# Optimization experiments

Measured on AMD Instinct MI355X. Metric: run time of the kernel, lower is better.

## Reference

```python
import jax, jax.numpy as jnp
import numpy as np

B, N, NB, E, H, A, K, D = 32, 512, 10, 1024, 256, 82, 4, 3


def setup_inputs() -> dict:
    key = jax.random.key(0)
    ks = iter(jax.random.split(key, 64))
    f = lambda shape: jax.random.normal(next(ks), shape, jnp.float32) * 0.05
    inp = {
        "atom_fea": jax.random.normal(next(ks), (B, N, A), jnp.float32),
        "bond_fea": jax.random.normal(next(ks), (B, E, 6), jnp.float32),
        "d_anb": jax.random.randint(next(ks), (B, N, NB), 0, N),
        "d_bnb": jax.random.randint(next(ks), (B, N, NB), 0, E),
        "d_nbs_mask": (jax.random.uniform(next(ks), (B, N, NB)) < 0.8).astype(jnp.float32),
        "d_mask": (jax.random.uniform(next(ks), (B, N)) < 0.9).astype(jnp.float32),
        "Wv": f((A, H)), "bv": f((H,)),
        "Wa_main": f((D, K, H, H)), "ba_main": f((D, K, H)),
        "Wa_super": f((D, K, H, H)), "ba_super": f((D, K, H)),
        "Wm": f((D, K, H, H)), "bm": f((D, K, H)),
        "Wbmm": f((D, K, H)), "bbmm": f((D, K)),
        "Wm2s": f((D, K * H, H)), "bm2s": f((D, H)),
        "Ws2m": f((D, H, H)), "bs2m": f((D, H)),
        "Wsup": f((D, H, H)), "bsup": f((D, H)),
        "Wzm1": f((D, H, H)), "bzm1": f((D, H)),
        "Wzm2": f((D, H, H)), "bzm2": f((D, H)),
        "Wzs1": f((D, H, H)), "bzs1": f((D, H)),
        "Wzs2": f((D, H, H)), "bzs2": f((D, H)),
        "Wu2": f((D, H + 6, H)), "bu2": f((D, H)),
        "Wu1": f((D, 2 * H, H)), "bu1": f((D, H)),
    }
    return inp


def mask_softmax(a, mask):
    a_max = jnp.max(a, -1, keepdims=True)
    e = jnp.exp(a - a_max) * mask
    return e / (jnp.sum(e, -1, keepdims=True) + 1e-6)


def _forward(atom_fea, bond_fea, d_nbs_mask, d_mask,
             Wv, bv, Wa_main, ba_main, Wa_super, ba_super, Wm, bm, Wbmm, bbmm,
             Wm2s, bm2s, Ws2m, bs2m, Wsup, bsup,
             Wzm1, bzm1, Wzm2, bzm2, Wzs1, bzs1, Wzs2, bzs2,
             Wu2, bu2, Wu1, bu1, d_anb, d_bnb):
    Bn = atom_fea.shape[0]
    bidx = jnp.arange(Bn)[:, None, None]
    # vertex embedding (default leaky_relu slope 0.01)
    vf = jax.nn.leaky_relu(atom_fea @ Wv + bv, 0.01)            # [B,N,H]
    sf = jnp.sum(vf * d_mask[:, :, None], axis=1, keepdims=True)  # [B,1,H]
    mask3 = d_nbs_mask[..., None]                               # [B,N,NB,1]
    for d in range(D):
        # --- multi-head main->super attention (vectorized over heads k) ---
        a_main = jnp.tanh(jnp.einsum('bnh,khj->bknj', vf, Wa_main[d]) + ba_main[d][None, :, None, :])
        a_super = jnp.tanh(jnp.einsum('boh,khj->bkoj', sf, Wa_super[d]) + ba_super[d][None, :, None, :])
        a = jnp.einsum('bknh,kh->bkn', a_main * a_super, Wbmm[d]) + bbmm[d][None, :, None]
        attn = mask_softmax(a, d_mask[:, None, :])               # [B,K,N]
        mvf = jnp.einsum('bnh,khj->bknj', vf, Wm[d]) + bm[d][None, :, None, :]
        m2s = jnp.einsum('bkn,bknh->bkh', attn, mvf).reshape(Bn, 1, K * H)
        main_to_super = jnp.tanh(m2s @ Wm2s[d] + bm2s[d])        # [B,1,H]
        # --- wln unit: gather neighbors, MLP, masked sum (slope 0.1) ---
        vnei = vf[bidx, d_anb]                                   # [B,N,NB,H]
        enei = bond_fea[bidx, d_bnb]                             # [B,N,NB,6]
        lnei = jnp.concatenate([vnei, enei], -1)                 # [B,N,NB,H+6]
        nei = jax.nn.leaky_relu(lnei @ Wu2[d] + bu2[d], 0.1)
        nei = jnp.sum(nei * mask3, axis=2)                       # [B,N,H]
        main_self = jax.nn.leaky_relu(jnp.concatenate([vf, nei], -1) @ Wu1[d] + bu1[d], 0.1)
        # --- GRU-style gated updates ---
        super_to_main = jnp.tanh(sf @ Ws2m[d] + bs2m[d])         # [B,1,H]
        super_self = jnp.tanh(sf @ Wsup[d] + bsup[d])            # [B,1,H]
        z_main = jax.nn.sigmoid(main_self @ Wzm1[d] + bzm1[d] + super_to_main @ Wzm2[d] + bzm2[d])
        vf = (1 - z_main) * main_self + z_main * super_to_main
        z_sup = jax.nn.sigmoid(super_self @ Wzs1[d] + bzs1[d] + main_to_super @ Wzs2[d] + bzs2[d])
        sf = (1 - z_sup) * super_self + z_sup * main_to_super    # [B,1,H]; sum over dim 1 is a no-op
    return vf, sf


def reference(atom_fea, bond_fea, d_anb, d_bnb, d_nbs_mask, d_mask,
              Wv, bv, Wa_main, ba_main, Wa_super, ba_super, Wm, bm, Wbmm, bbmm,
              Wm2s, bm2s, Ws2m, bs2m, Wsup, bsup,
              Wzm1, bzm1, Wzm2, bzm2, Wzs1, bzs1, Wzs2, bzs2,
              Wu2, bu2, Wu1, bu1):
    return _forward(atom_fea, bond_fea, d_nbs_mask, d_mask,
                    Wv, bv, Wa_main, ba_main, Wa_super, ba_super, Wm, bm, Wbmm, bbmm,
                    Wm2s, bm2s, Ws2m, bs2m, Wsup, bsup,
                    Wzm1, bzm1, Wzm2, bzm2, Wzs1, bzs1, Wzs2, bzs2,
                    Wu2, bu2, Wu1, bu1, d_anb, d_bnb)
```

## Files before the change

### kernel.cpp

```cpp
#include <hip/hip_runtime.h>
#include <hip/hip_bf16.h>

#define B_ 32
#define N_ 512
#define NB_ 10
#define E_ 1024
#define H_ 256
#define A_ 82
#define K_ 4
#define D_ 3
#define M_ (B_*N_)

typedef unsigned short u16;
typedef __attribute__((ext_vector_type(8))) short bf16x8;
typedef __attribute__((ext_vector_type(4))) float f32x4;

__device__ __forceinline__ float b2f(u16 u){
    unsigned int x = ((unsigned int)u) << 16;
    return __builtin_bit_cast(float, x);
}
__device__ __forceinline__ u16 f2b(float f){
    unsigned int x = __builtin_bit_cast(unsigned int, f);
    unsigned int lsb = (x >> 16) & 1u;
    x += 0x7fffu + lsb;
    return (u16)(x >> 16);
}
__device__ __forceinline__ float sigmoidf_(float x){ return 1.f/(1.f+expf(-x)); }

static constexpr int CVT_N[31] = {
    B_*E_*6, B_*N_*NB_, B_*N_,
    A_*H_, H_,
    D_*K_*H_*H_, D_*K_*H_, D_*K_*H_*H_, D_*K_*H_,
    D_*K_*H_*H_, D_*K_*H_, D_*K_*H_, D_*K_,
    D_*K_*H_*H_, D_*H_, D_*H_*H_, D_*H_,
    D_*H_*H_, D_*H_, D_*H_*H_, D_*H_,
    D_*H_*H_, D_*H_, D_*H_*H_, D_*H_,
    D_*H_*H_, D_*H_, D_*(H_+6)*H_, D_*H_,
    D_*2*H_*H_, D_*H_
};
struct Offs { long v[32]; };
static constexpr Offs mk_offs(){
    Offs o{}; o.v[0]=0;
    for(int i=0;i<31;i++) o.v[i+1]=o.v[i]+CVT_N[i];
    return o;
}
static constexpr Offs CVT_OFF = mk_offs();

struct Ptrs { const void* p[31]; };

__global__ void k_detect(const unsigned short* __restrict__ wv_raw, int* __restrict__ flag){
    float v = b2f(wv_raw[threadIdx.x]);
    bool plaus = (v==v) && (fabsf(v) < 100.0f);
    unsigned long long m = __ballot(plaus);
    if (threadIdx.x==0) *flag = (m == ~0ULL) ? 1 : 0;
}

__global__ void k_cvt(Ptrs ptrs, float* __restrict__ dst, const int* __restrict__ flag){
    int t = blockIdx.y;
    int n = CVT_N[t];
    int i4 = blockIdx.x*256 + threadIdx.x;
    if (i4*4 >= n) return;
    const void* src = ptrs.p[t];
    float4 o;
    if (*flag){
        ushort4 u = ((const ushort4*)src)[i4];
        o.x=b2f(u.x); o.y=b2f(u.y); o.z=b2f(u.z); o.w=b2f(u.w);
    } else {
        o = ((const float4*)src)[i4];
    }
    *(float4*)(dst + CVT_OFF.v[t] + (size_t)i4*4) = o;
}

__global__ void k_embed(const u16* __restrict__ atom, const float* __restrict__ Wv,
                        const float* __restrict__ bv, float* __restrict__ vf,
                        const int* __restrict__ flag){
    __shared__ float arow[A_];
    int row = blockIdx.x; int j = threadIdx.x;
    if (j < A_){
        if (*flag) arow[j] = b2f(atom[(size_t)row*A_ + j]);
        else       arow[j] = ((const float*)atom)[(size_t)row*A_ + j];
    }
    __syncthreads();
    float acc = bv[j];
    for(int a=0;a<A_;a++) acc += arow[a]*Wv[a*H_ + j];
    vf[(size_t)row*H_ + j] = acc > 0.f ? acc : 0.01f*acc;
}

__global__ void k_sf0(const float* __restrict__ vf, const float* __restrict__ dmask,
                      float* __restrict__ sf){
    int b = blockIdx.x, h = threadIdx.x;
    __shared__ float mk[N_];
    for(int n=threadIdx.x;n<N_;n+=256) mk[n] = dmask[b*N_+n];
    __syncthreads();
    float s=0.f;
    #pragma unroll 8
    for(int n=0;n<N_;n++) s += mk[n]*vf[((size_t)b*N_+n)*H_ + h];
    sf[b*H_+h]=s;
}

__global__ void k_s1(int d, const float* __restrict__ sf,
    const float* __restrict__ Was, const float* __restrict__ bas,
    const float* __restrict__ Wbmm,
    const float* __restrict__ Ws2m, const float* __restrict__ bs2m,
    const float* __restrict__ Wsup, const float* __restrict__ bsup,
    float* __restrict__ asw, float* __restrict__ s2m, float* __restrict__ ssf)
{
    int b = blockIdx.x, m = blockIdx.y, j = threadIdx.x;
    __shared__ float sfl[H_];
    sfl[j] = sf[b*H_+j];
    __syncthreads();
    const float* W; float bias;
    if (m < 4){ W = Was + (size_t)(d*K_+m)*H_*H_; bias = bas[(d*K_+m)*H_+j]; }
    else if (m==4){ W = Ws2m + (size_t)d*H_*H_; bias = bs2m[d*H_+j]; }
    else { W = Wsup + (size_t)d*H_*H_; bias = bsup[d*H_+j]; }
    float acc = bias;
    #pragma unroll 8
    for(int h=0;h<H_;h++) acc += sfl[h]*W[h*H_+j];
    float v = tanhf(acc);
    if (m < 4) asw[(b*K_+m)*H_+j] = v * Wbmm[(d*K_+m)*H_+j];
    else if (m==4) s2m[b*H_+j] = v;
    else ssf[b*H_+j] = v;
}

__global__ void k_s2(int d, const float* __restrict__ s2m,
    const float* __restrict__ Wzm2, const float* __restrict__ bzm2,
    float* __restrict__ stm2p)
{
    int b=blockIdx.x, c=blockIdx.y, j=threadIdx.x;
    __shared__ float xl[64];
    if (j<64) xl[j] = s2m[b*H_ + c*64 + j];
    __syncthreads();
    const float* W = Wzm2 + (size_t)d*H_*H_ + (size_t)(c*64)*H_;
    float acc = (c==0) ? bzm2[d*H_+j] : 0.f;
    #pragma unroll 8
    for(int h=0;h<64;h++) acc += xl[h]*W[h*H_+j];
    stm2p[((size_t)c*B_+b)*H_+j] = acc;
}

__device__ __forceinline__ void mfma_core_f32(const float* __restrict__ A,
    const float* __restrict__ W, f32x4 acc[2][8],
    u16* __restrict__ Als, u16* __restrict__ Ws)
{
    const int LSA = 40, LSW = 40;
    int tid = threadIdx.x;
    int lane = tid & 63, wave = tid >> 6;
    int wy = wave >> 1, wx = wave & 1;
    int quad = lane >> 4, l15 = lane & 15;
    #pragma unroll
    for(int mt=0;mt<2;mt++)
        #pragma unroll
        for(int nt=0;nt<8;nt++) acc[mt][nt] = (f32x4){0.f,0.f,0.f,0.f};
    int arow = tid >> 2;
    int ak8  = (tid & 3) * 8;
    for(int k0=0;k0<H_;k0+=32){
        float4 a0 = *(const float4*)(A + (size_t)arow*H_ + k0 + ak8);
        float4 a1 = *(const float4*)(A + (size_t)arow*H_ + k0 + ak8 + 4);
        union { u16 u[8]; bf16x8 v; } ua;
        ua.u[0]=f2b(a0.x); ua.u[1]=f2b(a0.y); ua.u[2]=f2b(a0.z); ua.u[3]=f2b(a0.w);
        ua.u[4]=f2b(a1.x); ua.u[5]=f2b(a1.y); ua.u[6]=f2b(a1.z); ua.u[7]=f2b(a1.w);
        *(bf16x8*)(Als + arow*LSA + ak8) = ua.v;
        union { u16 u[32]; bf16x8 v[4]; } uw;
        #pragma unroll
        for(int r=0;r<32;r++) uw.u[r] = f2b(W[(size_t)(k0+r)*H_ + tid]);
        #pragma unroll
        for(int c=0;c<4;c++) *(bf16x8*)(Ws + tid*LSW + c*8) = uw.v[c];
        __syncthreads();
        bf16x8 af[2], bfr[8];
        #pragma unroll
        for(int mt=0;mt<2;mt++)
            af[mt] = *(const bf16x8*)(Als + (wy*32+mt*16+l15)*LSA + quad*8);
        #pragma unroll
        for(int nt=0;nt<8;nt++)
            bfr[nt] = *(const bf16x8*)(Ws + (wx*128+nt*16+l15)*LSW + quad*8);
        #pragma unroll
        for(int mt=0;mt<2;mt++)
            #pragma unroll
            for(int nt=0;nt<8;nt++)
                acc[mt][nt] = __builtin_amdgcn_mfma_f32_16x16x32_bf16(
                    af[mt], bfr[nt], acc[mt][nt], 0,0,0);
        __syncthreads();
    }
}

__global__ __launch_bounds__(256) void k_gemm_big(int d, const float* __restrict__ vf,
    const float* __restrict__ Wa_main, const float* __restrict__ ba_main,
    const float* __restrict__ bbmm,
    const float* __restrict__ Wu2, const float* __restrict__ Wu1,
    const float* __restrict__ bu1,
    const float* __restrict__ asw, float* __restrict__ score,
    float* __restrict__ proj_u2, float* __restrict__ pu1a)
{
    __shared__ u16 Als[64*40];
    __shared__ u16 Ws[256*40];
    __shared__ float sred[64][33];
    int m0 = blockIdx.x*64;
    int seg = blockIdx.y;
    int b = m0 >> 9;
    const float* W;
    if (seg < 4)      W = Wa_main + ((size_t)(d*K_+seg))*H_*H_;
    else if (seg==4)  W = Wu2 + (size_t)d*(H_+6)*H_;
    else              W = Wu1 + (size_t)d*2*H_*H_;
    f32x4 acc[2][8];
    mfma_core_f32(vf + (size_t)m0*H_, W, acc, Als, Ws);
    int tid=threadIdx.x, lane=tid&63, wave=tid>>6;
    int wy=wave>>1, wx=wave&1, quad=lane>>4, l15=lane&15;
    if (seg < 4){
        const float* aswp = asw + (size_t)(b*K_+seg)*H_;
        const float* bap  = ba_main + (size_t)(d*K_+seg)*H_;
        float bbv[8], awv[8];
        #pragma unroll
        for(int nt=0;nt<8;nt++){
            int col = wx*128+nt*16+l15;
            bbv[nt]=bap[col]; awv[nt]=aswp[col];
        }
        #pragma unroll
        for(int mt=0;mt<2;mt++)
            #pragma unroll
            for(int r=0;r<4;r++){
                float p=0.f;
                #pragma unroll
                for(int nt=0;nt<8;nt++)
                    p += tanhf(acc[mt][nt][r]+bbv[nt])*awv[nt];
                int row = wy*32+mt*16+quad*4+r;
                sred[row][wx*16+l15] = p;
            }
        __syncthreads();
        if (tid < 64){
            float s=0.f;
            #pragma unroll 8
            for(int i=0;i<32;i++) s += sred[tid][i];
            score[(size_t)(b*K_+seg)*N_ + (m0&511) + tid] = s + bbmm[d*K_+seg];
        }
    } else if (seg==4){
        #pragma unroll
        for(int mt=0;mt<2;mt++)
            #pragma unroll
            for(int nt=0;nt<8;nt++){
                int col = wx*128+nt*16+l15;
                #pragma unroll
                for(int r=0;r<4;r++){
                    int row = m0 + wy*32+mt*16+quad*4+r;
                    proj_u2[(size_t)row*H_+col] = acc[mt][nt][r];
                }
            }
    } else {
        const float* bp = bu1 + d*H_;
        #pragma unroll
        for(int mt=0;mt<2;mt++)
            #pragma unroll
            for(int nt=0;nt<8;nt++){
                int col = wx*128+nt*16+l15;
                float bb = bp[col];
                #pragma unroll
                for(int r=0;r<4;r++){
                    int row = m0 + wy*32+mt*16+quad*4+r;
                    pu1a[(size_t)row*H_+col] = acc[mt][nt][r] + bb;
                }
            }
    }
}

__global__ __launch_bounds__(256) void k_mainself(int d, const float* __restrict__ nei,
    const float* __restrict__ Wu1, float* __restrict__ pu)
{
    __shared__ u16 Als[64*40];
    __shared__ u16 Ws[256*40];
    int m0 = blockIdx.x*64;
    const float* W = Wu1 + (size_t)d*2*H_*H_ + (size_t)H_*H_;
    f32x4 acc[2][8];
    mfma_core_f32(nei + (size_t)m0*H_, W, acc, Als, Ws);
    int tid=threadIdx.x, lane=tid&63, wave=tid>>6;
    int wy=wave>>1, wx=wave&1, quad=lane>>4, l15=lane&15;
    #pragma unroll
    for(int mt=0;mt<2;mt++)
        #pragma unroll
        for(int nt=0;nt<8;nt++){
            int col = wx*128+nt*16+l15;
            #pragma unroll
            for(int r=0;r<4;r++){
                int row = m0 + wy*32+mt*16+quad*4+r;
                float v = acc[mt][nt][r] + pu[(size_t)row*H_+col];
                v = v>0.f? v : 0.1f*v;
                pu[(size_t)row*H_+col] = v;
            }
        }
}

__global__ __launch_bounds__(256) void k_update(int d, const float* __restrict__ main_self,
    const float* __restrict__ Wzm1, const float* __restrict__ bzm1,
    const float* __restrict__ stm2p, const float* __restrict__ s2m, float* __restrict__ vf)
{
    __shared__ u16 Als[64*40];
    __shared__ u16 Ws[256*40];
    int m0 = blockIdx.x*64; int b = m0>>9;
    f32x4 acc[2][8];
    mfma_core_f32(main_self + (size_t)m0*H_, Wzm1 + (size_t)d*H_*H_, acc, Als, Ws);
    int tid=threadIdx.x, lane=tid&63, wave=tid>>6;
    int wy=wave>>1, wx=wave&1, quad=lane>>4, l15=lane&15;
    #pragma unroll
    for(int mt=0;mt<2;mt++)
        #pragma unroll
        for(int nt=0;nt<8;nt++){
            int col = wx*128+nt*16+l15;
            float bz = bzm1[d*H_+col];
            float st = stm2p[(size_t)(0*B_+b)*H_+col] + stm2p[(size_t)(1*B_+b)*H_+col]
                     + stm2p[(size_t)(2*B_+b)*H_+col] + stm2p[(size_t)(3*B_+b)*H_+col];
            float sm = s2m[b*H_+col];
            #pragma unroll
            for(int r=0;r<4;r++){
                int row = m0 + wy*32+mt*16+quad*4+r;
                float z = sigmoidf_(acc[mt][nt][r] + bz + st);
                float ms = main_self[(size_t)row*H_+col];
                vf[(size_t)row*H_+col] = (1.f-z)*ms + z*sm;
            }
        }
}

__global__ void k_softmax(float* __restrict__ score, const float* __restrict__ dmask,
                          float* __restrict__ sumattn){
    int b = blockIdx.x, k = blockIdx.y;
    int tid = threadIdx.x;
    __shared__ float sh[256];
    float* a = score + (size_t)(b*K_+k)*N_;
    float v0 = a[tid], v1 = a[tid+256];
    sh[tid]=fmaxf(v0,v1); __syncthreads();
    for(int s=128;s>0;s>>=1){ if(tid<s) sh[tid]=fmaxf(sh[tid],sh[tid+s]); __syncthreads(); }
    float m = sh[0]; __syncthreads();
    float e0 = expf(v0-m)*dmask[b*N_+tid], e1 = expf(v1-m)*dmask[b*N_+tid+256];
    sh[tid]=e0+e1; __syncthreads();
    for(int s=128;s>0;s>>=1){ if(tid<s) sh[tid]+=sh[tid+s]; __syncthreads(); }
    float S = sh[0];
    float inv = 1.f/(S+1e-6f);
    a[tid]=e0*inv; a[tid+256]=e1*inv;
    if(tid==0) sumattn[b*K_+k]=S*inv;
}

__global__ void k_t2(const float* __restrict__ attn, const float* __restrict__ vf,
                     float* __restrict__ tpart){
    int b=blockIdx.x, k=blockIdx.y, c=blockIdx.z, h=threadIdx.x;
    __shared__ float at[256];
    at[h] = attn[(size_t)(b*K_+k)*N_ + c*256 + h];
    __syncthreads();
    float acc=0.f;
    const float* vfp = vf + ((size_t)b*N_ + c*256)*H_ + h;
    #pragma unroll 8
    for(int n=0;n<256;n++) acc += at[n]*vfp[(size_t)n*H_];
    tpart[((size_t)(c*B_+b)*K_+k)*H_+h]=acc;
}

__global__ void k_m1(int d, const float* __restrict__ tpart, const float* __restrict__ sumattn,
    const float* __restrict__ Wm, const float* __restrict__ bm, float* __restrict__ m2s)
{
    int b=blockIdx.x, k=blockIdx.y, j=threadIdx.x;
    __shared__ float tl[H_];
    tl[j] = tpart[((size_t)(0*B_+b)*K_+k)*H_+j] + tpart[((size_t)(1*B_+b)*K_+k)*H_+j];
    __syncthreads();
    const float* W = Wm + (size_t)(d*K_+k)*H_*H_;
    float acc = sumattn[b*K_+k]*bm[(d*K_+k)*H_+j];
    #pragma unroll 8
    for(int h=0;h<H_;h++) acc += tl[h]*W[h*H_+j];
    m2s[(size_t)(b*K_+k)*H_+j]=acc;
}

__global__ void k_m2(int d, const float* __restrict__ m2s, const float* __restrict__ Wm2s,
                     float* __restrict__ mtsp)
{
    int b=blockIdx.x, c=blockIdx.y, j=threadIdx.x;
    __shared__ float xl[H_];
    xl[j]=m2s[(size_t)(b*K_+c)*H_+j];
    __syncthreads();
    const float* W = Wm2s + (size_t)d*(K_*H_)*H_ + (size_t)(c*H_)*H_;
    float acc=0.f;
    #pragma unroll 8
    for(int h=0;h<H_;h++) acc += xl[h]*W[h*H_+j];
    mtsp[((size_t)c*B_+b)*H_+j]=acc;
}

__global__ void k_mts(int d, const float* __restrict__ mtsp, const float* __restrict__ bm2s,
                      float* __restrict__ mts){
    int b=blockIdx.x, j=threadIdx.x;
    float acc = bm2s[d*H_+j];
    #pragma unroll
    for(int c=0;c<4;c++) acc += mtsp[((size_t)c*B_+b)*H_+j];
    mts[b*H_+j]=tanhf(acc);
}

__global__ void k_m3(int d, const float* __restrict__ ssf, const float* __restrict__ mts,
    const float* __restrict__ Wzs1, const float* __restrict__ Wzs2,
    float* __restrict__ p1, float* __restrict__ p2)
{
    int b=blockIdx.x, m=blockIdx.y, j=threadIdx.x;
    __shared__ float xl[H_];
    const float* x = m ? mts : ssf;
    xl[j]=x[b*H_+j];
    __syncthreads();
    const float* W = (m ? Wzs2 : Wzs1) + (size_t)d*H_*H_;
    float acc=0.f;
    #pragma unroll 8
    for(int h=0;h<H_;h++) acc += xl[h]*W[h*H_+j];
    (m ? p2 : p1)[b*H_+j]=acc;
}

__global__ void k_sfup(int d, const float* __restrict__ p1, const float* __restrict__ p2,
    const float* __restrict__ bzs1, const float* __restrict__ bzs2,
    const float* __restrict__ ssf, const float* __restrict__ mts, float* __restrict__ sf)
{
    int b=blockIdx.x, j=threadIdx.x;
    float z = sigmoidf_(p1[b*H_+j]+bzs1[d*H_+j]+p2[b*H_+j]+bzs2[d*H_+j]);
    sf[b*H_+j]=(1.f-z)*ssf[b*H_+j]+z*mts[b*H_+j];
}

__global__ void k_nei(int d, const int* __restrict__ anb, const int* __restrict__ bnb,
    const float* __restrict__ nbm, const float* __restrict__ bond,
    const float* __restrict__ Wu2, const float* __restrict__ bu2,
    const float* __restrict__ proj_u2, float* __restrict__ nei)
{
    __shared__ float W2s[6][256];
    __shared__ float bfeat[NB_][6];
    __shared__ int ai[NB_]; __shared__ int bi[NB_]; __shared__ float mk[NB_];
    int row = blockIdx.x; int b = row >> 9; int h = threadIdx.x;
    const float* W2 = Wu2 + (size_t)d*(H_+6)*H_ + (size_t)H_*H_;
    for(int i=h;i<6*H_;i+=256) W2s[i>>8][i&255] = W2[i];
    if (h<NB_){ ai[h]=anb[row*NB_+h]; bi[h]=bnb[row*NB_+h]; mk[h]=nbm[row*NB_+h]; }
    __syncthreads();
    if (h<NB_*6){ int jn=h/6, i=h-jn*6; bfeat[jn][i]=bond[((size_t)b*E_+bi[jn])*6+i]; }
    __syncthreads();
    float bu = bu2[d*H_+h];
    float acc=0.f;
    #pragma unroll
    for(int jn=0;jn<NB_;jn++){
        float v = proj_u2[((size_t)b*N_+ai[jn])*H_+h] + bu;
        #pragma unroll
        for(int i=0;i<6;i++) v += bfeat[jn][i]*W2s[i][h];
        v = v>0.f? v : 0.1f*v;
        acc += mk[jn]*v;
    }
    nei[(size_t)row*H_+h]=acc;
}

__global__ void k_out(const float* __restrict__ vf, const float* __restrict__ sf,
                      void* __restrict__ out, const int* __restrict__ flag){
    int idx = blockIdx.x*256 + threadIdx.x;
    const int total = M_*H_ + B_*H_;
    if (idx >= total) return;
    float v = (idx < M_*H_) ? vf[idx] : sf[idx - M_*H_];
    if (*flag) ((unsigned short*)out)[idx] = f2b(v);
    else       ((float*)out)[idx] = v;
}

extern "C" void kernel_launch(void* const* d_in, const int* in_sizes, int n_in,
                              void* d_out, int out_size, void* d_ws, size_t ws_size,
                              hipStream_t stream)
{
    const int* anb = (const int*)d_in[2];
    const int* bnb = (const int*)d_in[3];

    float* ws   = (float*)d_ws;
    int*   flag = (int*)ws;
    float* cvt  = ws + 64;
    float* p    = cvt + ((CVT_OFF.v[31] + 63) & ~63L);
    float* vf        = p; p += (size_t)M_*H_;
    float* proj_u2   = p; p += (size_t)M_*H_;
    float* proj_u1a  = p; p += (size_t)M_*H_;
    float* nei       = p; p += (size_t)M_*H_;
    float* sf        = p; p += B_*H_;
    float* score     = p; p += B_*K_*N_;
    float* sumattn   = p; p += B_*K_;
    float* asw       = p; p += B_*K_*H_;
    float* s2m       = p; p += B_*H_;
    float* ssf       = p; p += B_*H_;
    float* stm2p     = p; p += 4*B_*H_;
    float* tpart     = p; p += 2*B_*K_*H_;
    float* m2s       = p; p += B_*K_*H_;
    float* mtsp      = p; p += 4*B_*H_;
    float* mts       = p; p += B_*H_;
    float* p1        = p; p += B_*H_;
    float* p2        = p; p += B_*H_;

    const float* cBond = cvt + CVT_OFF.v[0];
    const float* cNbm  = cvt + CVT_OFF.v[1];
    const float* cDm   = cvt + CVT_OFF.v[2];
    const float* cWv   = cvt + CVT_OFF.v[3];
    const float* cbv   = cvt + CVT_OFF.v[4];
    const float* cWam  = cvt + CVT_OFF.v[5];
    const float* cbam  = cvt + CVT_OFF.v[6];
    const float* cWas  = cvt + CVT_OFF.v[7];
    const float* cbas  = cvt + CVT_OFF.v[8];
    const float* cWm   = cvt + CVT_OFF.v[9];
    const float* cbm   = cvt + CVT_OFF.v[10];
    const float* cWbmm = cvt + CVT_OFF.v[11];
    const float* cbbmm = cvt + CVT_OFF.v[12];
    const float* cWm2s = cvt + CVT_OFF.v[13];
    const float* cbm2s = cvt + CVT_OFF.v[14];
    const float* cWs2m = cvt + CVT_OFF.v[15];
    const float* cbs2m = cvt + CVT_OFF.v[16];
    const float* cWsup = cvt + CVT_OFF.v[17];
    const float* cbsup = cvt + CVT_OFF.v[18];
    const float* cWzm1 = cvt + CVT_OFF.v[19];
    const float* cbzm1 = cvt + CVT_OFF.v[20];
    const float* cWzm2 = cvt + CVT_OFF.v[21];
    const float* cbzm2 = cvt + CVT_OFF.v[22];
    const float* cWzs1 = cvt + CVT_OFF.v[23];
    const float* cbzs1 = cvt + CVT_OFF.v[24];
    const float* cWzs2 = cvt + CVT_OFF.v[25];
    const float* cbzs2 = cvt + CVT_OFF.v[26];
    const float* cWu2  = cvt + CVT_OFF.v[27];
    const float* cbu2  = cvt + CVT_OFF.v[28];
    const float* cWu1  = cvt + CVT_OFF.v[29];
    const float* cbu1  = cvt + CVT_OFF.v[30];

    Ptrs ptrs;
    {
        int idx[31] = {1,4,5,6,7,8,9,10,11,12,13,14,15,16,17,18,19,20,21,
                       22,23,24,25,26,27,28,29,30,31,32,33};
        for(int i=0;i<31;i++) ptrs.p[i] = d_in[idx[i]];
    }

    k_detect<<<1,64,0,stream>>>((const unsigned short*)d_in[6], flag);
    {
        int maxv4 = (D_*K_*H_*H_ + 3)/4;
        int gx = (maxv4 + 255)/256;
        k_cvt<<<dim3(gx,31),256,0,stream>>>(ptrs, cvt, flag);
    }

    k_embed<<<M_,256,0,stream>>>((const u16*)d_in[0], cWv, cbv, vf, flag);
    k_sf0<<<B_,256,0,stream>>>(vf, cDm, sf);
    for(int d=0; d<D_; d++){
        k_s1<<<dim3(B_,6),256,0,stream>>>(d, sf, cWas, cbas, cWbmm,
                                          cWs2m, cbs2m, cWsup, cbsup, asw, s2m, ssf);
        k_s2<<<dim3(B_,4),256,0,stream>>>(d, s2m, cWzm2, cbzm2, stm2p);
        k_gemm_big<<<dim3(M_/64,6),256,0,stream>>>(d, vf, cWam, cbam, cbbmm,
                                                   cWu2, cWu1, cbu1, asw, score,
                                                   proj_u2, proj_u1a);
        k_softmax<<<dim3(B_,K_),256,0,stream>>>(score, cDm, sumattn);
        k_t2<<<dim3(B_,K_,2),256,0,stream>>>(score, vf, tpart);
        k_m1<<<dim3(B_,K_),256,0,stream>>>(d, tpart, sumattn, cWm, cbm, m2s);
        k_m2<<<dim3(B_,4),256,0,stream>>>(d, m2s, cWm2s, mtsp);
        k_mts<<<B_,256,0,stream>>>(d, mtsp, cbm2s, mts);
        k_m3<<<dim3(B_,2),256,0,stream>>>(d, ssf, mts, cWzs1, cWzs2, p1, p2);
        k_sfup<<<B_,256,0,stream>>>(d, p1, p2, cbzs1, cbzs2, ssf, mts, sf);
        k_nei<<<M_,256,0,stream>>>(d, anb, bnb, cNbm, cBond, cWu2, cbu2, proj_u2, nei);
        k_mainself<<<M_/64,256,0,stream>>>(d, nei, cWu1, proj_u1a);
        k_update<<<M_/64,256,0,stream>>>(d, proj_u1a, cWzm1, cbzm1, stm2p, s2m, vf);
    }
    k_out<<<(M_*H_+B_*H_+255)/256,256,0,stream>>>(vf, sf, d_out, flag);
}
```

Baseline: 802.7 us.

## Pre-transpose GEMM weights to bf16 tiles and batch embed rows per block

A new pre-pass kernel transposes and converts every GEMM weight matrix into bf16 tiles laid out as [k-block][n][32]. The MFMA core can then load its weight tile with vector loads, where before each thread made 32 strided fp32 loads and conversions per k-step. Separately, the embedding kernel now handles 8 rows per block, so each Wv load is reused across those rows. This adds a transpose launch and a workspace buffer placed after the existing scratch; that works only if the workspace allocation is large enough.

```diff
diff --git a/kernel.cpp b/kernel.cpp
--- a/kernel.cpp
+++ b/kernel.cpp
@@ -71,19 +71,51 @@
     *(float4*)(dst + CVT_OFF.v[t] + (size_t)i4*4) = o;
 }
 
+__global__ void k_wt(const float* __restrict__ Wam, const float* __restrict__ Wu2,
+                     const float* __restrict__ Wu1, const float* __restrict__ Wzm1,
+                     u16* __restrict__ WT){
+    int mi = blockIdx.z;
+    const float* src;
+    if (mi<12)      src = Wam  + (size_t)mi*H_*H_;
+    else if (mi<15) src = Wu2  + (size_t)(mi-12)*(H_+6)*H_;
+    else if (mi<18) src = Wu1  + (size_t)(mi-15)*2*H_*H_;
+    else if (mi<21) src = Wu1  + (size_t)(mi-18)*2*H_*H_ + (size_t)H_*H_;
+    else            src = Wzm1 + (size_t)(mi-21)*H_*H_;
+    __shared__ float t[32][33];
+    int x = threadIdx.x, y = threadIdx.y;
+    int k0 = blockIdx.y*32, n0 = blockIdx.x*32;
+    for(int yy=y; yy<32; yy+=8) t[yy][x] = src[(size_t)(k0+yy)*H_ + n0+x];
+    __syncthreads();
+    u16* dst = WT + ((size_t)mi*8 + (k0>>5))*(256*32);
+    for(int yy=y; yy<32; yy+=8) dst[(size_t)(n0+yy)*32 + x] = f2b(t[x][yy]);
+}
+
 __global__ void k_embed(const u16* __restrict__ atom, const float* __restrict__ Wv,
                         const float* __restrict__ bv, float* __restrict__ vf,
                         const int* __restrict__ flag){
-    __shared__ float arow[A_];
-    int row = blockIdx.x; int j = threadIdx.x;
-    if (j < A_){
-        if (*flag) arow[j] = b2f(atom[(size_t)row*A_ + j]);
-        else       arow[j] = ((const float*)atom)[(size_t)row*A_ + j];
-    }
-    __syncthreads();
-    float acc = bv[j];
-    for(int a=0;a<A_;a++) acc += arow[a]*Wv[a*H_ + j];
-    vf[(size_t)row*H_ + j] = acc > 0.f ? acc : 0.01f*acc;
+    __shared__ float arow[8][A_];
+    int r0 = blockIdx.x*8; int j = threadIdx.x;
+    int fl = *flag;
+    for(int i=j;i<8*A_;i+=256){
+        int r=i/A_, a=i-r*A_;
+        arow[r][a] = fl ? b2f(atom[(size_t)(r0+r)*A_+a])
+                        : ((const float*)atom)[(size_t)(r0+r)*A_+a];
+    }
+    __syncthreads();
+    float acc[8];
+    float bj = bv[j];
+    #pragma unroll
+    for(int r=0;r<8;r++) acc[r]=bj;
+    for(int a=0;a<A_;a++){
+        float w = Wv[a*H_+j];
+        #pragma unroll
+        for(int r=0;r<8;r++) acc[r] += arow[r][a]*w;
+    }
+    #pragma unroll
+    for(int r=0;r<8;r++){
+        float v = acc[r];
+        vf[(size_t)(r0+r)*H_+j] = v>0.f ? v : 0.01f*v;
+    }
 }
 
 __global__ void k_sf0(const float* __restrict__ vf, const float* __restrict__ dmask,
@@ -137,8 +169,8 @@
     stm2p[((size_t)c*B_+b)*H_+j] = acc;
 }
 
-__device__ __forceinline__ void mfma_core_f32(const float* __restrict__ A,
-    const float* __restrict__ W, f32x4 acc[2][8],
+__device__ __forceinline__ void mfma_core_wt(const float* __restrict__ A,
+    const u16* __restrict__ WTg, f32x4 acc[2][8],
     u16* __restrict__ Als, u16* __restrict__ Ws)
 {
     const int LSA = 40, LSW = 40;
@@ -159,11 +191,10 @@
         ua.u[0]=f2b(a0.x); ua.u[1]=f2b(a0.y); ua.u[2]=f2b(a0.z); ua.u[3]=f2b(a0.w);
         ua.u[4]=f2b(a1.x); ua.u[5]=f2b(a1.y); ua.u[6]=f2b(a1.z); ua.u[7]=f2b(a1.w);
         *(bf16x8*)(Als + arow*LSA + ak8) = ua.v;
-        union { u16 u[32]; bf16x8 v[4]; } uw;
-        #pragma unroll
-        for(int r=0;r<32;r++) uw.u[r] = f2b(W[(size_t)(k0+r)*H_ + tid]);
-        #pragma unroll
-        for(int c=0;c<4;c++) *(bf16x8*)(Ws + tid*LSW + c*8) = uw.v[c];
+        const u16* wsrc = WTg + (size_t)(k0>>5)*(256*32) + tid*32;
+        #pragma unroll
+        for(int c=0;c<4;c++)
+            *(bf16x8*)(Ws + tid*LSW + c*8) = *(const bf16x8*)(wsrc + c*8);
         __syncthreads();
         bf16x8 af[2], bfr[8];
         #pragma unroll
@@ -183,10 +214,8 @@
 }
 
 __global__ __launch_bounds__(256) void k_gemm_big(int d, const float* __restrict__ vf,
-    const float* __restrict__ Wa_main, const float* __restrict__ ba_main,
-    const float* __restrict__ bbmm,
-    const float* __restrict__ Wu2, const float* __restrict__ Wu1,
-    const float* __restrict__ bu1,
+    const u16* __restrict__ WT, const float* __restrict__ ba_main,
+    const float* __restrict__ bbmm, const float* __restrict__ bu1,
     const float* __restrict__ asw, float* __restrict__ score,
     float* __restrict__ proj_u2, float* __restrict__ pu1a)
 {
@@ -196,12 +225,12 @@
     int m0 = blockIdx.x*64;
     int seg = blockIdx.y;
     int b = m0 >> 9;
-    const float* W;
-    if (seg < 4)      W = Wa_main + ((size_t)(d*K_+seg))*H_*H_;
-    else if (seg==4)  W = Wu2 + (size_t)d*(H_+6)*H_;
-    else              W = Wu1 + (size_t)d*2*H_*H_;
+    int mi;
+    if (seg < 4)      mi = d*4+seg;
+    else if (seg==4)  mi = 12+d;
+    else              mi = 15+d;
     f32x4 acc[2][8];
-    mfma_core_f32(vf + (size_t)m0*H_, W, acc, Als, Ws);
+    mfma_core_wt(vf + (size_t)m0*H_, WT + (size_t)mi*H_*H_, acc, Als, Ws);
     int tid=threadIdx.x, lane=tid&63, wave=tid>>6;
     int wy=wave>>1, wx=wave&1, quad=lane>>4, l15=lane&15;
     if (seg < 4){
@@ -261,14 +290,13 @@
 }
 
 __global__ __launch_bounds__(256) void k_mainself(int d, const float* __restrict__ nei,
-    const float* __restrict__ Wu1, float* __restrict__ pu)
+    const u16* __restrict__ WT, float* __restrict__ pu)
 {
     __shared__ u16 Als[64*40];
     __shared__ u16 Ws[256*40];
     int m0 = blockIdx.x*64;
-    const float* W = Wu1 + (size_t)d*2*H_*H_ + (size_t)H_*H_;
     f32x4 acc[2][8];
-    mfma_core_f32(nei + (size_t)m0*H_, W, acc, Als, Ws);
+    mfma_core_wt(nei + (size_t)m0*H_, WT + (size_t)(18+d)*H_*H_, acc, Als, Ws);
     int tid=threadIdx.x, lane=tid&63, wave=tid>>6;
     int wy=wave>>1, wx=wave&1, quad=lane>>4, l15=lane&15;
     #pragma unroll
@@ -287,14 +315,14 @@
 }
 
 __global__ __launch_bounds__(256) void k_update(int d, const float* __restrict__ main_self,
-    const float* __restrict__ Wzm1, const float* __restrict__ bzm1,
+    const u16* __restrict__ WT, const float* __restrict__ bzm1,
     const float* __restrict__ stm2p, const float* __restrict__ s2m, float* __restrict__ vf)
 {
     __shared__ u16 Als[64*40];
     __shared__ u16 Ws[256*40];
     int m0 = blockIdx.x*64; int b = m0>>9;
     f32x4 acc[2][8];
-    mfma_core_f32(main_self + (size_t)m0*H_, Wzm1 + (size_t)d*H_*H_, acc, Als, Ws);
+    mfma_core_wt(main_self + (size_t)m0*H_, WT + (size_t)(21+d)*H_*H_, acc, Als, Ws);
     int tid=threadIdx.x, lane=tid&63, wave=tid>>6;
     int wy=wave>>1, wx=wave&1, quad=lane>>4, l15=lane&15;
     #pragma unroll
@@ -476,6 +504,7 @@
     float* mts       = p; p += B_*H_;
     float* p1        = p; p += B_*H_;
     float* p2        = p; p += B_*H_;
+    u16*   WT        = (u16*)p;
 
     const float* cBond = cvt + CVT_OFF.v[0];
     const float* cNbm  = cvt + CVT_OFF.v[1];
@@ -522,16 +551,16 @@
         int gx = (maxv4 + 255)/256;
         k_cvt<<<dim3(gx,31),256,0,stream>>>(ptrs, cvt, flag);
     }
-
-    k_embed<<<M_,256,0,stream>>>((const u16*)d_in[0], cWv, cbv, vf, flag);
+    k_wt<<<dim3(8,8,24),dim3(32,8),0,stream>>>(cWam, cWu2, cWu1, cWzm1, WT);
+
+    k_embed<<<M_/8,256,0,stream>>>((const u16*)d_in[0], cWv, cbv, vf, flag);
     k_sf0<<<B_,256,0,stream>>>(vf, cDm, sf);
     for(int d=0; d<D_; d++){
         k_s1<<<dim3(B_,6),256,0,stream>>>(d, sf, cWas, cbas, cWbmm,
                                           cWs2m, cbs2m, cWsup, cbsup, asw, s2m, ssf);
         k_s2<<<dim3(B_,4),256,0,stream>>>(d, s2m, cWzm2, cbzm2, stm2p);
-        k_gemm_big<<<dim3(M_/64,6),256,0,stream>>>(d, vf, cWam, cbam, cbbmm,
-                                                   cWu2, cWu1, cbu1, asw, score,
-                                                   proj_u2, proj_u1a);
+        k_gemm_big<<<dim3(M_/64,6),256,0,stream>>>(d, vf, WT, cbam, cbbmm, cbu1,
+                                                   asw, score, proj_u2, proj_u1a);
         k_softmax<<<dim3(B_,K_),256,0,stream>>>(score, cDm, sumattn);
         k_t2<<<dim3(B_,K_,2),256,0,stream>>>(score, vf, tpart);
         k_m1<<<dim3(B_,K_),256,0,stream>>>(d, tpart, sumattn, cWm, cbm, m2s);
@@ -540,8 +569,8 @@
         k_m3<<<dim3(B_,2),256,0,stream>>>(d, ssf, mts, cWzs1, cWzs2, p1, p2);
         k_sfup<<<B_,256,0,stream>>>(d, p1, p2, cbzs1, cbzs2, ssf, mts, sf);
         k_nei<<<M_,256,0,stream>>>(d, anb, bnb, cNbm, cBond, cWu2, cbu2, proj_u2, nei);
-        k_mainself<<<M_/64,256,0,stream>>>(d, nei, cWu1, proj_u1a);
-        k_update<<<M_/64,256,0,stream>>>(d, proj_u1a, cWzm1, cbzm1, stm2p, s2m, vf);
+        k_mainself<<<M_/64,256,0,stream>>>(d, nei, WT, proj_u1a);
+        k_update<<<M_/64,256,0,stream>>>(d, proj_u1a, WT, cbzm1, stm2p, s2m, vf);
     }
     k_out<<<(M_*H_+B_*H_+255)/256,256,0,stream>>>(vf, sf, d_out, flag);
 }
```

New measurement: 746.0 us. 7.1% less time.
